# Kernel tuning notes

Measured on AMD Instinct MI355X. Metric: run time of the kernel, lower is better.

The kernel has to match this reference:

```python
import jax, jax.numpy as jnp
import numpy as np

B = 4_194_304
N_STATES = 21

# normal_ranges_I_R02_Gripper_Pot, indexed by cycle_state-1 -> (min, max)
_R02 = np.full((N_STATES, 2), (11500.0, 12000.0), dtype=np.float32)
_R02[3] = (6400.0, 12000.0)   # state 4
_R02[4:8] = (6000.0, 12000.0) # states 5-8
# normal_ranges_I_R03_Gripper_Pot
_R03 = np.full((N_STATES, 2), (2200.0, 2500.0), dtype=np.float32)
_R03[7] = (2200.0, 13000.0)   # state 8
R02 = jnp.asarray(_R02)
R03 = jnp.asarray(_R03)


def setup_inputs() -> dict:
    key = jax.random.key(0)
    k1, k2, k3, k4, k5, k6 = jax.random.split(key, 6)
    # sensor targets on realistic scale, anomaly class in {100,...,700}
    t0 = jax.random.randint(k2, (B,), 2000, 13000, dtype=jnp.int32)
    t1 = jax.random.randint(k3, (B,), 2000, 13000, dtype=jnp.int32)
    t2 = (jax.random.randint(k4, (B,), 0, 7, dtype=jnp.int32) + 1) * 100
    targets = jnp.stack([t0, t1, t2], axis=1)  # [B, 3] int32
    # predictions near target scale
    inputs = jax.random.normal(k1, (B, 3), dtype=jnp.float32) * 100.0 + 8000.0
    cycle_states = jax.random.randint(k5, (B,), 1, N_STATES + 1, dtype=jnp.int32)
    weights = jax.random.uniform(k6, (7,), dtype=jnp.float32) + 0.5
    return {"inputs": inputs, "targets": targets,
            "cycle_states": cycle_states, "weights": weights}


def _range_penalty(v, lo, hi):
    # (v-lo)^2 if v < lo, (v-hi)^2 if v > hi, else 0
    below = jnp.where(v < lo, (v - lo) ** 2, 0.0)
    above = jnp.where(v > hi, (v - hi) ** 2, 0.0)
    return below + above


def reference(inputs, targets, cycle_states, weights):
    tf = targets.astype(jnp.float32)                 # targets.long() -> float math
    # class_to_index: {100:0,...,700:6} == t//100 - 1 (vectorized gather)
    mapped = targets[:, 2] // 100 - 1                # [B] int
    sw = weights[mapped]                             # [B] sample weights

    diff2 = (inputs[:, :2] - tf[:, :2]) ** 2         # [B, 2]
    weighted_loss_sensors = (sw[:, None] * diff2).mean(axis=1).mean()

    weighted_loss_anomaly = (sw * (inputs[:, 2] - tf[:, 2]) ** 2).mean()

    idx = cycle_states - 1                           # [B] in [0, 21)
    r02 = R02[idx]                                   # [B, 2]
    r03 = R03[idx]                                   # [B, 2]
    pen = (_range_penalty(tf[:, 0], r02[:, 0], r02[:, 1])
           + _range_penalty(tf[:, 1], r03[:, 0], r03[:, 1])).sum()

    return weighted_loss_sensors + weighted_loss_anomaly + pen
```

## Files before the change

### kernel.cpp

```cpp
#include <hip/hip_runtime.h>


#define NTHREADS 256

#define INV_B 2.384185791015625e-07f

typedef float f32x4 __attribute__((ext_vector_type(4)));
typedef int   i32x4 __attribute__((ext_vector_type(4)));

__global__ __launch_bounds__(NTHREADS) void wmse_main(
    const f32x4* __restrict__ in4,
    const i32x4* __restrict__ tg4,
    const i32x4* __restrict__ st4,
    const float* __restrict__ weights,
    float*       __restrict__ out)
{
    __shared__ float w[8];
    if (threadIdx.x < 7) w[threadIdx.x] = weights[threadIdx.x];
    __syncthreads();

    const int q = blockIdx.x * NTHREADS + threadIdx.x;

    f32x4 a  = __builtin_nontemporal_load(in4 + 3 * q + 0);
    f32x4 b  = __builtin_nontemporal_load(in4 + 3 * q + 1);
    f32x4 c  = __builtin_nontemporal_load(in4 + 3 * q + 2);
    i32x4 ta = __builtin_nontemporal_load(tg4 + 3 * q + 0);
    i32x4 tb = __builtin_nontemporal_load(tg4 + 3 * q + 1);
    i32x4 tc = __builtin_nontemporal_load(tg4 + 3 * q + 2);
    i32x4 s  = __builtin_nontemporal_load(st4 + q);

    float fin[12] = {a[0], a[1], a[2], a[3], b[0], b[1], b[2], b[3],
                     c[0], c[1], c[2], c[3]};
    int   tgt[12] = {ta[0], ta[1], ta[2], ta[3], tb[0], tb[1], tb[2], tb[3],
                     tc[0], tc[1], tc[2], tc[3]};
    int    st[4]  = {s[0], s[1], s[2], s[3]};

    double acc = 0.0;
    #pragma unroll
    for (int r = 0; r < 4; ++r) {
        const float i0 = fin[3 * r + 0];
        const float i1 = fin[3 * r + 1];
        const float i2 = fin[3 * r + 2];
        const int  t2i = tgt[3 * r + 2];
        const float t0 = (float)tgt[3 * r + 0];
        const float t1 = (float)tgt[3 * r + 1];
        const float t2 = (float)t2i;

        const float sw = w[t2i / 100 - 1];

        const float d0 = (i0 - t0) * (i0 - t0);
        const float d1 = (i1 - t1) * (i1 - t1);
        const float d2 = (i2 - t2) * (i2 - t2);
        const float mse = sw * (0.5f * (d0 + d1) + d2);

        const int idx = st[r] - 1;
        const float lo02 = (idx == 3) ? 6400.0f
                         : ((idx >= 4 && idx <= 7) ? 6000.0f : 11500.0f);
        const float hi02 = 12000.0f;
        const float lo03 = 2200.0f;
        const float hi03 = (idx == 7) ? 13000.0f : 2500.0f;

        float p = 0.0f;
        {
            const float dl = t0 - lo02, dh = t0 - hi02;
            p += (t0 < lo02) ? dl * dl : 0.0f;
            p += (t0 > hi02) ? dh * dh : 0.0f;
        }
        {
            const float dl = t1 - lo03, dh = t1 - hi03;
            p += (t1 < lo03) ? dl * dl : 0.0f;
            p += (t1 > hi03) ? dh * dh : 0.0f;
        }

        acc += (double)(mse * INV_B) + (double)p;
    }

    #pragma unroll
    for (int o = 32; o > 0; o >>= 1) acc += __shfl_down(acc, o, 64);
    __shared__ double sacc[NTHREADS / 64];
    const int lane = threadIdx.x & 63;
    const int wave = threadIdx.x >> 6;
    if (lane == 0) sacc[wave] = acc;
    __syncthreads();
    if (threadIdx.x == 0) {
        double ssum = 0.0;
        #pragma unroll
        for (int wv = 0; wv < NTHREADS / 64; ++wv) ssum += sacc[wv];
        atomicAdd(out, (float)ssum);
    }
}

extern "C" void kernel_launch(void* const* d_in, const int* in_sizes, int n_in,
                              void* d_out, int out_size, void* d_ws, size_t ws_size,
                              hipStream_t stream) {
    const float* inputs  = (const float*)d_in[0];
    const int*   targets = (const int*)  d_in[1];
    const int*   states  = (const int*)  d_in[2];
    const float* weights = (const float*)d_in[3];

    const int B = in_sizes[2];
    const int nquads = B / 4;
    const int nblocks = nquads / NTHREADS;

    float* out = (float*)d_out;

    hipMemsetAsync(out, 0, sizeof(float), stream);

    wmse_main<<<nblocks, NTHREADS, 0, stream>>>(
        (const f32x4*)inputs, (const i32x4*)targets, (const i32x4*)states,
        weights, out);
}
```

Baseline: 171.5 us.

## Process four quads per thread, switch to float accumulation, drop nontemporal loads

Each thread now handles four 16-byte quads, strided by block size, so a quarter as many blocks launch and there are fewer global atomics. All loads are issued before any compute to raise memory-level parallelism. Accumulation and the reduction move from double to float, which cuts FP64 work and shuffle cost but may lose precision, since the penalty terms are large. The nontemporal load hints are replaced with plain loads.

```diff
diff --git a/kernel.cpp b/kernel.cpp
--- a/kernel.cpp
+++ b/kernel.cpp
@@ -2,6 +2,7 @@
 
 
 #define NTHREADS 256
+#define QPT 4
 
 #define INV_B 2.384185791015625e-07f
 
@@ -19,74 +20,86 @@
     if (threadIdx.x < 7) w[threadIdx.x] = weights[threadIdx.x];
     __syncthreads();
 
-    const int q = blockIdx.x * NTHREADS + threadIdx.x;
+    const int base = blockIdx.x * (NTHREADS * QPT) + threadIdx.x;
 
-    f32x4 a  = __builtin_nontemporal_load(in4 + 3 * q + 0);
-    f32x4 b  = __builtin_nontemporal_load(in4 + 3 * q + 1);
-    f32x4 c  = __builtin_nontemporal_load(in4 + 3 * q + 2);
-    i32x4 ta = __builtin_nontemporal_load(tg4 + 3 * q + 0);
-    i32x4 tb = __builtin_nontemporal_load(tg4 + 3 * q + 1);
-    i32x4 tc = __builtin_nontemporal_load(tg4 + 3 * q + 2);
-    i32x4 s  = __builtin_nontemporal_load(st4 + q);
+    f32x4 A[QPT][3];
+    i32x4 T[QPT][3];
+    i32x4 S[QPT];
+    #pragma unroll
+    for (int j = 0; j < QPT; ++j) {
+        const int q = base + j * NTHREADS;
+        A[j][0] = in4[3 * q + 0];
+        A[j][1] = in4[3 * q + 1];
+        A[j][2] = in4[3 * q + 2];
+        T[j][0] = tg4[3 * q + 0];
+        T[j][1] = tg4[3 * q + 1];
+        T[j][2] = tg4[3 * q + 2];
+        S[j]    = st4[q];
+    }
 
-    float fin[12] = {a[0], a[1], a[2], a[3], b[0], b[1], b[2], b[3],
-                     c[0], c[1], c[2], c[3]};
-    int   tgt[12] = {ta[0], ta[1], ta[2], ta[3], tb[0], tb[1], tb[2], tb[3],
-                     tc[0], tc[1], tc[2], tc[3]};
-    int    st[4]  = {s[0], s[1], s[2], s[3]};
+    float acc = 0.0f;
+    #pragma unroll
+    for (int j = 0; j < QPT; ++j) {
+        float fin[12] = {A[j][0][0], A[j][0][1], A[j][0][2], A[j][0][3],
+                         A[j][1][0], A[j][1][1], A[j][1][2], A[j][1][3],
+                         A[j][2][0], A[j][2][1], A[j][2][2], A[j][2][3]};
+        int   tgt[12] = {T[j][0][0], T[j][0][1], T[j][0][2], T[j][0][3],
+                         T[j][1][0], T[j][1][1], T[j][1][2], T[j][1][3],
+                         T[j][2][0], T[j][2][1], T[j][2][2], T[j][2][3]};
+        int    st[4]  = {S[j][0], S[j][1], S[j][2], S[j][3]};
 
-    double acc = 0.0;
-    #pragma unroll
-    for (int r = 0; r < 4; ++r) {
-        const float i0 = fin[3 * r + 0];
-        const float i1 = fin[3 * r + 1];
-        const float i2 = fin[3 * r + 2];
-        const int  t2i = tgt[3 * r + 2];
-        const float t0 = (float)tgt[3 * r + 0];
-        const float t1 = (float)tgt[3 * r + 1];
-        const float t2 = (float)t2i;
+        #pragma unroll
+        for (int r = 0; r < 4; ++r) {
+            const float i0 = fin[3 * r + 0];
+            const float i1 = fin[3 * r + 1];
+            const float i2 = fin[3 * r + 2];
+            const int  t2i = tgt[3 * r + 2];
+            const float t0 = (float)tgt[3 * r + 0];
+            const float t1 = (float)tgt[3 * r + 1];
+            const float t2 = (float)t2i;
 
-        const float sw = w[t2i / 100 - 1];
+            const float sw = w[t2i / 100 - 1];
 
-        const float d0 = (i0 - t0) * (i0 - t0);
-        const float d1 = (i1 - t1) * (i1 - t1);
-        const float d2 = (i2 - t2) * (i2 - t2);
-        const float mse = sw * (0.5f * (d0 + d1) + d2);
+            const float d0 = (i0 - t0) * (i0 - t0);
+            const float d1 = (i1 - t1) * (i1 - t1);
+            const float d2 = (i2 - t2) * (i2 - t2);
+            const float mse = sw * (0.5f * (d0 + d1) + d2);
 
-        const int idx = st[r] - 1;
-        const float lo02 = (idx == 3) ? 6400.0f
-                         : ((idx >= 4 && idx <= 7) ? 6000.0f : 11500.0f);
-        const float hi02 = 12000.0f;
-        const float lo03 = 2200.0f;
-        const float hi03 = (idx == 7) ? 13000.0f : 2500.0f;
+            const int idx = st[r] - 1;
+            const float lo02 = (idx == 3) ? 6400.0f
+                             : ((idx >= 4 && idx <= 7) ? 6000.0f : 11500.0f);
+            const float hi02 = 12000.0f;
+            const float lo03 = 2200.0f;
+            const float hi03 = (idx == 7) ? 13000.0f : 2500.0f;
 
-        float p = 0.0f;
-        {
-            const float dl = t0 - lo02, dh = t0 - hi02;
-            p += (t0 < lo02) ? dl * dl : 0.0f;
-            p += (t0 > hi02) ? dh * dh : 0.0f;
+            float p = 0.0f;
+            {
+                const float dl = t0 - lo02, dh = t0 - hi02;
+                p += (t0 < lo02) ? dl * dl : 0.0f;
+                p += (t0 > hi02) ? dh * dh : 0.0f;
+            }
+            {
+                const float dl = t1 - lo03, dh = t1 - hi03;
+                p += (t1 < lo03) ? dl * dl : 0.0f;
+                p += (t1 > hi03) ? dh * dh : 0.0f;
+            }
+
+            acc += mse * INV_B + p;
         }
-        {
-            const float dl = t1 - lo03, dh = t1 - hi03;
-            p += (t1 < lo03) ? dl * dl : 0.0f;
-            p += (t1 > hi03) ? dh * dh : 0.0f;
-        }
-
-        acc += (double)(mse * INV_B) + (double)p;
     }
 
     #pragma unroll
     for (int o = 32; o > 0; o >>= 1) acc += __shfl_down(acc, o, 64);
-    __shared__ double sacc[NTHREADS / 64];
+    __shared__ float sacc[NTHREADS / 64];
     const int lane = threadIdx.x & 63;
     const int wave = threadIdx.x >> 6;
     if (lane == 0) sacc[wave] = acc;
     __syncthreads();
     if (threadIdx.x == 0) {
-        double ssum = 0.0;
+        float ssum = 0.0f;
         #pragma unroll
         for (int wv = 0; wv < NTHREADS / 64; ++wv) ssum += sacc[wv];
-        atomicAdd(out, (float)ssum);
+        atomicAdd(out, ssum);
     }
 }
 
@@ -100,7 +113,7 @@
 
     const int B = in_sizes[2];
     const int nquads = B / 4;
-    const int nblocks = nquads / NTHREADS;
+    const int nblocks = nquads / (NTHREADS * QPT);
 
     float* out = (float*)d_out;
 
```

After: 141.5 us. 17.5% less time.
